# Optimization experiments

Hardware: AMD Instinct MI355X
Metric: run time of the kernel (lower is better)

## Reference

```python
import jax, jax.numpy as jnp
import numpy as np

B, S, H = 4, 2048, 2048
NH, NKV, HD = 8, 4, 256
WINDOW = 1024
ROPE_BASE = 10000.0
SCALE = 256.0 ** -0.5  # query_pre_attn_scalar ** -0.5


def setup_inputs() -> dict:
    key = jax.random.key(0)
    ks = jax.random.split(key, 6)
    s = 0.02
    return {
        "hidden_states": jax.random.normal(ks[0], (B, S, H), jnp.float32),
        "positions": jnp.tile(jnp.arange(S, dtype=jnp.int32), (B, 1)),
        "Wq": jax.random.normal(ks[1], (H, NH * HD), jnp.float32) * s,
        "bq": jnp.zeros((NH * HD,), jnp.float32),
        "Wk": jax.random.normal(ks[2], (H, NKV * HD), jnp.float32) * s,
        "bk": jnp.zeros((NKV * HD,), jnp.float32),
        "Wv": jax.random.normal(ks[3], (H, NKV * HD), jnp.float32) * s,
        "bv": jnp.zeros((NKV * HD,), jnp.float32),
        "Wo": jax.random.normal(ks[4], (NH * HD, H), jnp.float32) * s,
    }


def _rope_neox(pos, x):
    # pos: [B,S] int; x: [B,S,nh,HD]
    half = HD // 2
    inv_freq = 1.0 / (ROPE_BASE ** (jnp.arange(half, dtype=jnp.float32) / half))
    freqs = pos[..., None].astype(jnp.float32) * inv_freq  # [B,S,half]
    cos = jnp.cos(freqs)[:, :, None, :]
    sin = jnp.sin(freqs)[:, :, None, :]
    x1, x2 = jnp.split(x, 2, axis=-1)
    return jnp.concatenate([x1 * cos - x2 * sin, x2 * cos + x1 * sin], axis=-1)


def reference(hidden_states, positions, Wq, bq, Wk, bk, Wv, bv, Wo):
    q = (hidden_states @ Wq + bq).reshape(B, S, NH, HD)
    k = (hidden_states @ Wk + bk).reshape(B, S, NKV, HD)
    v = (hidden_states @ Wv + bv).reshape(B, S, NKV, HD)
    q = _rope_neox(positions, q)
    k = _rope_neox(positions, k)
    # GQA: repeat kv heads
    rep = NH // NKV
    k = jnp.repeat(k, rep, axis=2)
    v = jnp.repeat(v, rep, axis=2)
    scores = jnp.einsum('bqhd,bkhd->bhqk', q, k) * SCALE
    i = jnp.arange(S)[:, None]
    j = jnp.arange(S)[None, :]
    mask = (j <= i) & (j > i - WINDOW)  # causal + sliding window
    scores = jnp.where(mask[None, None], scores, jnp.float32(-1e30))
    probs = jax.nn.softmax(scores, axis=-1)
    attn = jnp.einsum('bhqk,bkhd->bqhd', probs, v).reshape(B, S, NH * HD)
    return attn @ Wo
```

## Files before the change

### kernel.cpp

```cpp
#include <hip/hip_runtime.h>

#define B_ 4
#define S_ 2048
#define H_ 2048
#define NH_ 8
#define NKV_ 4
#define HD_ 256
#define WINDOW_ 1024
#define SCALE_ 0.0625f

typedef __bf16 bf16x8 __attribute__((ext_vector_type(8)));
typedef float f32x4 __attribute__((ext_vector_type(4)));

__device__ __forceinline__ unsigned short f2bf(float f) {
  union { float f; unsigned u; } v; v.f = f;
  unsigned r = v.u + 0x7fffu + ((v.u >> 16) & 1u);
  return (unsigned short)(r >> 16);
}
__device__ __forceinline__ float bf2f(unsigned short h) {
  union { unsigned u; float f; } v; v.u = ((unsigned)h) << 16;
  return v.f;
}

__device__ __forceinline__ f32x4 mfma16(bf16x8 a, bf16x8 b, f32x4 c) {
  return __builtin_amdgcn_mfma_f32_16x16x32_bf16(a, b, c, 0, 0, 0);
}

#define GLOAD16(gsrc, ldst)                                                     \
  __builtin_amdgcn_global_load_lds(                                             \
      (const __attribute__((address_space(1))) void*)(gsrc),                    \
      (__attribute__((address_space(3))) void*)(ldst), 16, 0, 0)

#define FENCE asm volatile("" ::: "memory")
#define BAR __builtin_amdgcn_s_barrier()
#define WAIT_LGKM0 asm volatile("s_waitcnt lgkmcnt(0)" ::: "memory")

__global__ void f32_to_bf16(const float* __restrict__ in,
                            unsigned short* __restrict__ out, int n4) {
  int idx = blockIdx.x * blockDim.x + threadIdx.x;
  int stride = gridDim.x * blockDim.x;
  for (; idx < n4; idx += stride) {
    float4 v = reinterpret_cast<const float4*>(in)[idx];
    ushort4 o;
    o.x = f2bf(v.x); o.y = f2bf(v.y); o.z = f2bf(v.z); o.w = f2bf(v.w);
    reinterpret_cast<ushort4*>(out)[idx] = o;
  }
}

__global__ void transpose_w(const float* __restrict__ in,
                            unsigned short* __restrict__ out, int R, int C) {
  __shared__ unsigned short t[32][33];
  int r0 = blockIdx.x * 32, c0 = blockIdx.y * 32;
  int tx = threadIdx.x & 31, ty = threadIdx.x >> 5;
#pragma unroll
  for (int i = 0; i < 4; ++i)
    t[ty * 4 + i][tx] = f2bf(in[(size_t)(r0 + ty * 4 + i) * C + c0 + tx]);
  __syncthreads();
#pragma unroll
  for (int i = 0; i < 4; ++i)
    out[(size_t)(c0 + ty * 4 + i) * R + r0 + tx] = t[tx][ty * 4 + i];
}


#define SA(buf, kt, ha)                                                        \
  { _Pragma("unroll") for (int ii = 0; ii < 2; ++ii) {                         \
      int row_ = ii * 128 + (ha) * 64 + (tid >> 3);                            \
      GLOAD16(gA + (((size_t)(m0 + row_)) << 11) + ((kt) << 6) +               \
                  ((((tid & 7) ^ ((tid >> 3) & 7))) << 3),                     \
              lds + (buf) * 65536 + ((ii * 128 + (ha) * 64 + wid * 8) << 7)); } }

#define SB(buf, kt, hb)                                                        \
  { _Pragma("unroll") for (int ii = 0; ii < 2; ++ii) {                         \
      int row_ = ii * 128 + (hb) * 64 + (tid >> 3);                            \
      GLOAD16(gB + (((size_t)(n0 + row_)) << 11) + ((kt) << 6) +               \
                  ((((tid & 7) ^ ((tid >> 3) & 7))) << 3),                     \
              lds + (buf) * 65536 + 32768 +                                    \
                  ((ii * 128 + (hb) * 64 + wid * 8) << 7)); } }

#define RDA(buf, qa)                                                           \
  { _Pragma("unroll") for (int m = 0; m < 4; ++m)                              \
      _Pragma("unroll") for (int ks = 0; ks < 2; ++ks)                         \
        afr[m][ks] = *reinterpret_cast<const bf16x8*>(                         \
            lds + (buf) * 65536 +                                              \
            ((wm * 128 + (qa) * 64 + m * 16 + lc) << 7) +                      \
            ((((ks * 4 + lg) ^ (lc & 7))) << 4)); }

#define RDB(buf, qb, dst)                                                      \
  { _Pragma("unroll") for (int n = 0; n < 2; ++n)                              \
      _Pragma("unroll") for (int ks = 0; ks < 2; ++ks)                         \
        dst[n][ks] = *reinterpret_cast<const bf16x8*>(                         \
            lds + (buf) * 65536 + 32768 +                                      \
            ((wn * 64 + (qb) * 32 + n * 16 + lc) << 7) +                       \
            ((((ks * 4 + lg) ^ (lc & 7))) << 4)); }

#define MM(qa, qb, bsrc)                                                       \
  { __builtin_amdgcn_s_setprio(1);                                             \
    _Pragma("unroll") for (int m = 0; m < 4; ++m)                              \
      _Pragma("unroll") for (int n = 0; n < 2; ++n)                            \
        _Pragma("unroll") for (int ks = 0; ks < 2; ++ks)                       \
          acc[qa][qb][m][n] =                                                  \
              mfma16(afr[m][ks], bsrc[n][ks], acc[qa][qb][m][n]);              \
    __builtin_amdgcn_s_setprio(0); }

template <int OUT_F32>
__global__ __launch_bounds__(512, 2) void gemm256(
    const unsigned short* __restrict__ gA, const unsigned short* __restrict__ gB,
    const float* __restrict__ bias, void* __restrict__ Cout) {
  extern __shared__ __align__(16) char lds[];
  const int tid = threadIdx.x, lane = tid & 63, wid = tid >> 6;
  const int lc = lane & 15, lg = lane >> 4;
  const int wm = wid >> 2, wn = wid & 3;
  const int c = blockIdx.x & 7, bi = blockIdx.x >> 3;
  const int mt = ((c & 3) << 3) + (bi & 7);
  const int nt = ((c >> 2) << 2) + (bi >> 3);
  const int m0 = mt * 256, n0 = nt * 256;

  f32x4 acc[2][2][4][2];
#pragma unroll
  for (int qa = 0; qa < 2; ++qa)
#pragma unroll
    for (int qb = 0; qb < 2; ++qb)
#pragma unroll
      for (int m = 0; m < 4; ++m)
#pragma unroll
        for (int n = 0; n < 2; ++n) acc[qa][qb][m][n] = f32x4{0.f, 0.f, 0.f, 0.f};

  SA(0, 0, 0); SB(0, 0, 0); SB(0, 0, 1); SA(0, 0, 1);
  SA(1, 1, 0); SB(1, 1, 0); SB(1, 1, 1);
  asm volatile("s_waitcnt vmcnt(6)" ::: "memory");
  FENCE; BAR;

  bf16x8 afr[4][2], b0r[2][2], b1r[2][2];
  for (int t = 0; t < 32; ++t) {
    const int b = t & 1;
    const int t1 = (t + 1) & 31, t2 = (t + 2) & 31;
    const int bn = (t + 1) & 1;
    RDA(b, 0); RDB(b, 0, b0r);
    SA(bn, t1, 1);
    FENCE; BAR;
    MM(0, 0, b0r);
    WAIT_LGKM0; FENCE; BAR;
    RDB(b, 1, b1r);
    SA(b, t2, 0);
    FENCE; BAR;
    MM(0, 1, b1r);
    WAIT_LGKM0; FENCE; BAR;
    RDA(b, 1);
    SB(b, t2, 0);
    FENCE; BAR;
    MM(1, 0, b0r);
    WAIT_LGKM0; FENCE; BAR;
    SB(b, t2, 1);
    FENCE; BAR;
    MM(1, 1, b1r);
    asm volatile("s_waitcnt vmcnt(6)" ::: "memory");
    FENCE; BAR;
  }
  asm volatile("s_waitcnt vmcnt(0)" ::: "memory");

#pragma unroll
  for (int qa = 0; qa < 2; ++qa)
#pragma unroll
    for (int qb = 0; qb < 2; ++qb)
#pragma unroll
      for (int m = 0; m < 4; ++m)
#pragma unroll
        for (int n = 0; n < 2; ++n) {
          const int gcol = n0 + wn * 64 + qb * 32 + n * 16 + lc;
          const float bv = bias ? bias[gcol] : 0.f;
          const int grow = m0 + wm * 128 + qa * 64 + m * 16 + lg * 4;
#pragma unroll
          for (int r = 0; r < 4; ++r) {
            float v = acc[qa][qb][m][n][r] + bv;
            if (OUT_F32)
              reinterpret_cast<float*>(Cout)[(size_t)(grow + r) * 2048 + gcol] = v;
            else
              reinterpret_cast<unsigned short*>(Cout)[(size_t)(grow + r) * 2048 + gcol] = f2bf(v);
          }
        }
}

__global__ void rope_kernel(const unsigned short* __restrict__ in,
                            const int* __restrict__ pos,
                            unsigned short* __restrict__ out, int nh) {
  int idx = blockIdx.x * 256 + threadIdx.x;
  int d = idx & 127;
  int bs = idx >> 7;
  int b = bs >> 11, s = bs & 2047;
  float p = (float)pos[bs];
  float inv = __expf(-(float)d * (9.210340371976184f / 128.f));
  float fr = p * inv;
  float cs, sn;
  sincosf(fr, &sn, &cs);
  const unsigned short* ib = in + (size_t)bs * 2048 + d;
  unsigned short* ob = out + ((size_t)b * nh * S_ + s) * HD_ + d;
  for (int hh = 0; hh < nh; ++hh) {
    float x1 = bf2f(ib[hh * HD_]);
    float x2 = bf2f(ib[hh * HD_ + 128]);
    ob[(size_t)hh * S_ * HD_] = f2bf(x1 * cs - x2 * sn);
    ob[(size_t)hh * S_ * HD_ + 128] = f2bf(x2 * cs + x1 * sn);
  }
}

__global__ void transpose_v(const unsigned short* __restrict__ in,
                            unsigned short* __restrict__ out) {
  __shared__ unsigned short t[32][33];
  int s0 = blockIdx.x * 32, d0 = blockIdx.y * 32;
  int bh = blockIdx.z;
  int b = bh >> 2, hh = bh & 3;
  int tx = threadIdx.x & 31, ty = threadIdx.x >> 5;
#pragma unroll
  for (int i = 0; i < 4; ++i)
    t[ty * 4 + i][tx] =
        in[(size_t)(b * S_ + s0 + ty * 4 + i) * 2048 + 1024 + hh * 256 + d0 + tx];
  __syncthreads();
#pragma unroll
  for (int i = 0; i < 4; ++i)
    out[((size_t)(b * NKV_ + hh) * HD_ + d0 + ty * 4 + i) * S_ + s0 + tx] =
        t[tx][ty * 4 + i];
}


#define STAGE_KV(bf, kv0)                                                      \
  { _Pragma("unroll") for (int i = 0; i < 2; ++i) {                            \
      int chunk = i * 512 + tid; int row = chunk >> 5, o = chunk & 31;         \
      GLOAD16(Kg0 + (size_t)((kv0) + row) * HD_ + (o ^ (row & 7)) * 8,         \
              (char*)&Kl[bf][0] + (i * 512 + wid * 64) * 16); }                \
    _Pragma("unroll") for (int i = 0; i < 2; ++i) {                            \
      int chunk = i * 512 + tid; int row = chunk >> 2, o = chunk & 3;          \
      GLOAD16(Vg0 + (size_t)row * S_ + (kv0) + (o ^ ((row >> 1) & 3)) * 8,     \
              (char*)&Vl[bf][0] + (i * 512 + wid * 64) * 16); } }

__global__ __launch_bounds__(512, 4) void attn_kernel(
    const unsigned short* __restrict__ Q, const unsigned short* __restrict__ K,
    const unsigned short* __restrict__ VT, unsigned short* __restrict__ O) {
  __shared__ __align__(16) unsigned short Kl[2][32 * 256];
  __shared__ __align__(16) unsigned short Vl[2][256 * 32];
  __shared__ __align__(16) unsigned short Pl[8][16 * 40];

  const int tid = threadIdx.x;
  const int lane = tid & 63, wid = tid >> 6;
  const int wq = wid & 3;
  const int ho = wid >> 2;
  const int lc = lane & 15, lg = lane >> 4;
  const int qt = 31 - blockIdx.x;
  const int kvh = blockIdx.y, b = blockIdx.z;
  const int h = kvh * 2 + ho;
  const int q0 = qt * 64;

  bf16x8 qf[8];
  const unsigned short* Qbase =
      Q + (((size_t)(b * NH_ + h)) * S_ + (q0 + wq * 16 + lc)) * HD_;
#pragma unroll
  for (int ds = 0; ds < 8; ++ds)
    qf[ds] = *reinterpret_cast<const bf16x8*>(Qbase + ds * 32 + lg * 8);

  f32x4 acc[16];
#pragma unroll
  for (int i = 0; i < 16; ++i) acc[i] = f32x4{0.f, 0.f, 0.f, 0.f};
  float m_r[4], l_r[4];
#pragma unroll
  for (int r = 0; r < 4; ++r) { m_r[r] = -1e30f; l_r[r] = 0.f; }

  const unsigned short* Kg0 = K + ((size_t)(b * NKV_ + kvh)) * S_ * HD_;
  const unsigned short* Vg0 = VT + ((size_t)(b * NKV_ + kvh)) * HD_ * S_;

  int jlo = q0 - (WINDOW_ - 1);
  if (jlo < 0) jlo = 0;
  const int jt_lo = jlo >> 5;
  const int jt_hi = (q0 + 63) >> 5;
  const int ibase = q0 + wq * 16 + lg * 4;

  STAGE_KV(0, jt_lo * 32);
  int bf = 0;
  for (int jt = jt_lo; jt <= jt_hi; ++jt) {
    const int kv0 = jt * 32;
    if (jt < jt_hi) {
      STAGE_KV(bf ^ 1, (jt + 1) * 32);
      asm volatile("s_waitcnt vmcnt(4)" ::: "memory");
    } else {
      asm volatile("s_waitcnt vmcnt(0)" ::: "memory");
    }
    FENCE;
    __syncthreads();

    f32x4 sf[2];
    __builtin_amdgcn_s_setprio(1);
#pragma unroll
    for (int ct = 0; ct < 2; ++ct) {
      f32x4 s{0.f, 0.f, 0.f, 0.f};
      int j = ct * 16 + lc;
#pragma unroll
      for (int ds = 0; ds < 8; ++ds) {
        int g = ds * 4 + lg;
        const bf16x8 kf = *reinterpret_cast<const bf16x8*>(
            (const char*)&Kl[bf][0] + (j * 512 + ((g ^ (j & 7)) * 16)));
        s = mfma16(qf[ds], kf, s);
      }
      sf[ct] = s;
    }
    __builtin_amdgcn_s_setprio(0);

    float pmax[4];
#pragma unroll
    for (int r = 0; r < 4; ++r) pmax[r] = -1e30f;
#pragma unroll
    for (int ct = 0; ct < 2; ++ct) {
      int j = kv0 + ct * 16 + lc;
#pragma unroll
      for (int r = 0; r < 4; ++r) {
        int irow = ibase + r;
        bool ok = (j <= irow) && (j > irow - WINDOW_);
        pmax[r] = fmaxf(pmax[r], ok ? sf[ct][r] * SCALE_ : -1e30f);
      }
    }
#pragma unroll
    for (int r = 0; r < 4; ++r) {
#pragma unroll
      for (int msk = 1; msk <= 8; msk <<= 1)
        pmax[r] = fmaxf(pmax[r], __shfl_xor(pmax[r], msk));
    }
    float dmax = 0.f;
#pragma unroll
    for (int r = 0; r < 4; ++r) dmax = fmaxf(dmax, pmax[r] - m_r[r]);
    if (__any(dmax > 8.0f)) {
#pragma unroll
      for (int r = 0; r < 4; ++r) {
        float mn = fmaxf(m_r[r], pmax[r]);
        float a = __expf(m_r[r] - mn);
        m_r[r] = mn;
        l_r[r] *= a;
#pragma unroll
        for (int dt = 0; dt < 16; ++dt) acc[dt][r] *= a;
      }
    }
    float lsum[4];
#pragma unroll
    for (int r = 0; r < 4; ++r) lsum[r] = 0.f;
#pragma unroll
    for (int ct = 0; ct < 2; ++ct) {
      int j = kv0 + ct * 16 + lc;
#pragma unroll
      for (int r = 0; r < 4; ++r) {
        int irow = ibase + r;
        bool ok = (j <= irow) && (j > irow - WINDOW_);
        float p = ok ? __expf(sf[ct][r] * SCALE_ - m_r[r]) : 0.f;
        lsum[r] += p;
        Pl[wid][(lg * 4 + r) * 40 + ct * 16 + lc] = f2bf(p);
      }
    }
#pragma unroll
    for (int r = 0; r < 4; ++r) {
#pragma unroll
      for (int msk = 1; msk <= 8; msk <<= 1) lsum[r] += __shfl_xor(lsum[r], msk);
      l_r[r] += lsum[r];
    }
    WAIT_LGKM0;
    const bf16x8 pa = *reinterpret_cast<const bf16x8*>(&Pl[wid][lc * 40 + lg * 8]);
    __builtin_amdgcn_s_setprio(1);
#pragma unroll
    for (int dt = 0; dt < 16; ++dt) {
      int d = dt * 16 + lc;
      const bf16x8 vf = *reinterpret_cast<const bf16x8*>(
          (const char*)&Vl[bf][0] + (d * 64 + ((lg ^ ((d >> 1) & 3)) * 16)));
      acc[dt] = mfma16(pa, vf, acc[dt]);
    }
    __builtin_amdgcn_s_setprio(0);
    WAIT_LGKM0; FENCE;
    __syncthreads();
    bf ^= 1;
  }

  const int srow = q0 + wq * 16 + lg * 4;
#pragma unroll
  for (int dt = 0; dt < 16; ++dt) {
#pragma unroll
    for (int r = 0; r < 4; ++r) {
      float o = acc[dt][r] / l_r[r];
      O[(size_t)(b * S_ + srow + r) * (NH_ * HD_) + h * HD_ + dt * 16 + lc] =
          f2bf(o);
    }
  }
}

extern "C" void kernel_launch(void* const* d_in, const int* in_sizes, int n_in,
                              void* d_out, int out_size, void* d_ws,
                              size_t ws_size, hipStream_t stream) {
  (void)in_sizes; (void)n_in; (void)out_size; (void)ws_size;
  const float* hs = (const float*)d_in[0];
  const int* pos = (const int*)d_in[1];
  const float* Wq = (const float*)d_in[2];
  const float* bq = (const float*)d_in[3];
  const float* Wk = (const float*)d_in[4];
  const float* bk = (const float*)d_in[5];
  const float* Wv = (const float*)d_in[6];
  const float* bv = (const float*)d_in[7];
  const float* Wo = (const float*)d_in[8];
  float* out = (float*)d_out;

  char* ws = (char*)d_ws;
  const size_t MB = 1024 * 1024;
  unsigned short* hs_bf = (unsigned short*)(ws + 0);
  unsigned short* WqT   = (unsigned short*)(ws + 32 * MB);
  unsigned short* WkvT  = (unsigned short*)(ws + 40 * MB);
  unsigned short* WoT   = (unsigned short*)(ws + 48 * MB);
  unsigned short* Qflat = (unsigned short*)(ws + 56 * MB);
  unsigned short* KVflat= (unsigned short*)(ws + 88 * MB);
  unsigned short* Qatt  = (unsigned short*)(ws + 120 * MB);
  unsigned short* Katt  = (unsigned short*)(ws + 152 * MB);
  unsigned short* VTt   = (unsigned short*)(ws + 168 * MB);
  float* bias_kv = (float*)(ws + 120 * MB);
  unsigned short* attnb = (unsigned short*)(ws + 0);

  hipFuncSetAttribute(reinterpret_cast<const void*>(gemm256<0>),
                      hipFuncAttributeMaxDynamicSharedMemorySize, 131072);
  hipFuncSetAttribute(reinterpret_cast<const void*>(gemm256<1>),
                      hipFuncAttributeMaxDynamicSharedMemorySize, 131072);

  f32_to_bf16<<<2048, 256, 0, stream>>>(hs, hs_bf, (B_ * S_ * H_) / 4);
  transpose_w<<<dim3(H_ / 32, (NH_ * HD_) / 32), 256, 0, stream>>>(Wq, WqT, H_, NH_ * HD_);
  transpose_w<<<dim3(H_ / 32, (NKV_ * HD_) / 32), 256, 0, stream>>>(Wk, WkvT, H_, NKV_ * HD_);
  transpose_w<<<dim3(H_ / 32, (NKV_ * HD_) / 32), 256, 0, stream>>>(Wv, WkvT + 1024 * 2048, H_, NKV_ * HD_);
  transpose_w<<<dim3((NH_ * HD_) / 32, H_ / 32), 256, 0, stream>>>(Wo, WoT, NH_ * HD_, H_);
  hipMemcpyAsync(bias_kv, bk, 1024 * sizeof(float), hipMemcpyDeviceToDevice, stream);
  hipMemcpyAsync(bias_kv + 1024, bv, 1024 * sizeof(float), hipMemcpyDeviceToDevice, stream);

  gemm256<0><<<256, 512, 131072, stream>>>(hs_bf, WqT, bq, Qflat);
  gemm256<0><<<256, 512, 131072, stream>>>(hs_bf, WkvT, bias_kv, KVflat);

  rope_kernel<<<(B_ * S_ * 128) / 256, 256, 0, stream>>>(Qflat, pos, Qatt, NH_);
  rope_kernel<<<(B_ * S_ * 128) / 256, 256, 0, stream>>>(KVflat, pos, Katt, NKV_);
  transpose_v<<<dim3(S_ / 32, HD_ / 32, B_ * NKV_), 256, 0, stream>>>(KVflat, VTt);

  attn_kernel<<<dim3(32, 4, 4), 512, 0, stream>>>(Qatt, Katt, VTt, attnb);

  gemm256<1><<<256, 512, 131072, stream>>>(attnb, WoT, nullptr, out);
}
```

Before: 647.7 us.

## Fuse QKV projections into one GEMM and widen attention KV tiles to 64

Concatenates Wq, Wk and Wv into one transposed weight and runs a single 512-block GEMM producing a 4096-wide QKV buffer, replacing two separate projection launches. Rope and V-transpose kernels now read from the fused buffer. The attention kernel moves to dynamic LDS with 64-key tiles instead of 32, halving the number of loop iterations and barriers. Blocks are remapped so each XCD handles a fixed batch/head pair, but the larger LDS footprint drops occupancy to one block per CU.

```diff
diff --git a/kernel.cpp b/kernel.cpp
--- a/kernel.cpp
+++ b/kernel.cpp
@@ -102,7 +102,7 @@
               mfma16(afr[m][ks], bsrc[n][ks], acc[qa][qb][m][n]);              \
     __builtin_amdgcn_s_setprio(0); }
 
-template <int OUT_F32>
+template <int OUT_F32, int NTILES>
 __global__ __launch_bounds__(512, 2) void gemm256(
     const unsigned short* __restrict__ gA, const unsigned short* __restrict__ gB,
     const float* __restrict__ bias, void* __restrict__ Cout) {
@@ -110,9 +110,10 @@
   const int tid = threadIdx.x, lane = tid & 63, wid = tid >> 6;
   const int lc = lane & 15, lg = lane >> 4;
   const int wm = wid >> 2, wn = wid & 3;
+  const int N_ = NTILES * 256;
   const int c = blockIdx.x & 7, bi = blockIdx.x >> 3;
   const int mt = ((c & 3) << 3) + (bi & 7);
-  const int nt = ((c >> 2) << 2) + (bi >> 3);
+  const int nt = ((c >> 2) * (NTILES / 2)) + (bi >> 3);
   const int m0 = mt * 256, n0 = nt * 256;
 
   f32x4 acc[2][2][4][2];
@@ -173,16 +174,17 @@
           for (int r = 0; r < 4; ++r) {
             float v = acc[qa][qb][m][n][r] + bv;
             if (OUT_F32)
-              reinterpret_cast<float*>(Cout)[(size_t)(grow + r) * 2048 + gcol] = v;
+              reinterpret_cast<float*>(Cout)[(size_t)(grow + r) * N_ + gcol] = v;
             else
-              reinterpret_cast<unsigned short*>(Cout)[(size_t)(grow + r) * 2048 + gcol] = f2bf(v);
+              reinterpret_cast<unsigned short*>(Cout)[(size_t)(grow + r) * N_ + gcol] = f2bf(v);
           }
         }
 }
 
 __global__ void rope_kernel(const unsigned short* __restrict__ in,
                             const int* __restrict__ pos,
-                            unsigned short* __restrict__ out, int nh) {
+                            unsigned short* __restrict__ out, int nh,
+                            int colbase) {
   int idx = blockIdx.x * 256 + threadIdx.x;
   int d = idx & 127;
   int bs = idx >> 7;
@@ -192,7 +194,7 @@
   float fr = p * inv;
   float cs, sn;
   sincosf(fr, &sn, &cs);
-  const unsigned short* ib = in + (size_t)bs * 2048 + d;
+  const unsigned short* ib = in + (size_t)bs * 4096 + colbase + d;
   unsigned short* ob = out + ((size_t)b * nh * S_ + s) * HD_ + d;
   for (int hh = 0; hh < nh; ++hh) {
     float x1 = bf2f(ib[hh * HD_]);
@@ -212,7 +214,7 @@
 #pragma unroll
   for (int i = 0; i < 4; ++i)
     t[ty * 4 + i][tx] =
-        in[(size_t)(b * S_ + s0 + ty * 4 + i) * 2048 + 1024 + hh * 256 + d0 + tx];
+        in[(size_t)(b * S_ + s0 + ty * 4 + i) * 4096 + 3072 + hh * 256 + d0 + tx];
   __syncthreads();
 #pragma unroll
   for (int i = 0; i < 4; ++i)
@@ -221,32 +223,33 @@
 }
 
 
-#define STAGE_KV(bf, kv0)                                                      \
-  { _Pragma("unroll") for (int i = 0; i < 2; ++i) {                            \
+#define STAGE_KV(bfb, kv0)                                                     \
+  { _Pragma("unroll") for (int i = 0; i < 4; ++i) {                            \
       int chunk = i * 512 + tid; int row = chunk >> 5, o = chunk & 31;         \
       GLOAD16(Kg0 + (size_t)((kv0) + row) * HD_ + (o ^ (row & 7)) * 8,         \
-              (char*)&Kl[bf][0] + (i * 512 + wid * 64) * 16); }                \
-    _Pragma("unroll") for (int i = 0; i < 2; ++i) {                            \
-      int chunk = i * 512 + tid; int row = chunk >> 2, o = chunk & 3;          \
-      GLOAD16(Vg0 + (size_t)row * S_ + (kv0) + (o ^ ((row >> 1) & 3)) * 8,     \
-              (char*)&Vl[bf][0] + (i * 512 + wid * 64) * 16); } }
-
-__global__ __launch_bounds__(512, 4) void attn_kernel(
+              lds + (bfb) * 32768 + chunk * 16); }                             \
+    _Pragma("unroll") for (int i = 0; i < 4; ++i) {                            \
+      int chunk = i * 512 + tid; int row = chunk >> 3, o = chunk & 7;          \
+      GLOAD16(Vg0 + (size_t)row * S_ + (kv0) + (o ^ (row & 7)) * 8,            \
+              lds + 65536 + (bfb) * 32768 + chunk * 16); } }
+
+__global__ __launch_bounds__(512, 1) void attn_kernel(
     const unsigned short* __restrict__ Q, const unsigned short* __restrict__ K,
     const unsigned short* __restrict__ VT, unsigned short* __restrict__ O) {
-  __shared__ __align__(16) unsigned short Kl[2][32 * 256];
-  __shared__ __align__(16) unsigned short Vl[2][256 * 32];
-  __shared__ __align__(16) unsigned short Pl[8][16 * 40];
+  extern __shared__ __align__(16) char lds[];
 
   const int tid = threadIdx.x;
   const int lane = tid & 63, wid = tid >> 6;
   const int wq = wid & 3;
   const int ho = wid >> 2;
   const int lc = lane & 15, lg = lane >> 4;
-  const int qt = 31 - blockIdx.x;
-  const int kvh = blockIdx.y, b = blockIdx.z;
+  const int xcd = blockIdx.x & 7, g = blockIdx.x >> 3;
+  const int pair = xcd + ((g >> 5) << 3);
+  const int qt = 31 - (g & 31);
+  const int kvh = pair & 3, b = pair >> 2;
   const int h = kvh * 2 + ho;
   const int q0 = qt * 64;
+  unsigned short* Pl = (unsigned short*)(lds + 131072 + wid * 2304);
 
   bf16x8 qf[8];
   const unsigned short* Qbase =
@@ -267,34 +270,34 @@
 
   int jlo = q0 - (WINDOW_ - 1);
   if (jlo < 0) jlo = 0;
-  const int jt_lo = jlo >> 5;
-  const int jt_hi = (q0 + 63) >> 5;
+  const int jt_lo = jlo >> 6;
+  const int jt_hi = q0 >> 6;
   const int ibase = q0 + wq * 16 + lg * 4;
 
-  STAGE_KV(0, jt_lo * 32);
+  STAGE_KV(0, jt_lo * 64);
   int bf = 0;
   for (int jt = jt_lo; jt <= jt_hi; ++jt) {
-    const int kv0 = jt * 32;
+    const int kv0 = jt * 64;
     if (jt < jt_hi) {
-      STAGE_KV(bf ^ 1, (jt + 1) * 32);
-      asm volatile("s_waitcnt vmcnt(4)" ::: "memory");
+      STAGE_KV(bf ^ 1, (jt + 1) * 64);
+      asm volatile("s_waitcnt vmcnt(8)" ::: "memory");
     } else {
       asm volatile("s_waitcnt vmcnt(0)" ::: "memory");
     }
     FENCE;
     __syncthreads();
 
-    f32x4 sf[2];
+    f32x4 sf[4];
     __builtin_amdgcn_s_setprio(1);
 #pragma unroll
-    for (int ct = 0; ct < 2; ++ct) {
+    for (int ct = 0; ct < 4; ++ct) {
       f32x4 s{0.f, 0.f, 0.f, 0.f};
       int j = ct * 16 + lc;
 #pragma unroll
       for (int ds = 0; ds < 8; ++ds) {
-        int g = ds * 4 + lg;
+        int gg = ds * 4 + lg;
         const bf16x8 kf = *reinterpret_cast<const bf16x8*>(
-            (const char*)&Kl[bf][0] + (j * 512 + ((g ^ (j & 7)) * 16)));
+            lds + bf * 32768 + j * 512 + ((gg ^ (j & 7)) * 16));
         s = mfma16(qf[ds], kf, s);
       }
       sf[ct] = s;
@@ -305,7 +308,7 @@
 #pragma unroll
     for (int r = 0; r < 4; ++r) pmax[r] = -1e30f;
 #pragma unroll
-    for (int ct = 0; ct < 2; ++ct) {
+    for (int ct = 0; ct < 4; ++ct) {
       int j = kv0 + ct * 16 + lc;
 #pragma unroll
       for (int r = 0; r < 4; ++r) {
@@ -338,7 +341,7 @@
 #pragma unroll
     for (int r = 0; r < 4; ++r) lsum[r] = 0.f;
 #pragma unroll
-    for (int ct = 0; ct < 2; ++ct) {
+    for (int ct = 0; ct < 4; ++ct) {
       int j = kv0 + ct * 16 + lc;
 #pragma unroll
       for (int r = 0; r < 4; ++r) {
@@ -346,7 +349,7 @@
         bool ok = (j <= irow) && (j > irow - WINDOW_);
         float p = ok ? __expf(sf[ct][r] * SCALE_ - m_r[r]) : 0.f;
         lsum[r] += p;
-        Pl[wid][(lg * 4 + r) * 40 + ct * 16 + lc] = f2bf(p);
+        Pl[(lg * 4 + r) * 72 + ct * 16 + lc] = f2bf(p);
       }
     }
 #pragma unroll
@@ -356,14 +359,18 @@
       l_r[r] += lsum[r];
     }
     WAIT_LGKM0;
-    const bf16x8 pa = *reinterpret_cast<const bf16x8*>(&Pl[wid][lc * 40 + lg * 8]);
+    bf16x8 pa0 = *reinterpret_cast<const bf16x8*>(&Pl[lc * 72 + lg * 8]);
+    bf16x8 pa1 = *reinterpret_cast<const bf16x8*>(&Pl[lc * 72 + 32 + lg * 8]);
     __builtin_amdgcn_s_setprio(1);
 #pragma unroll
     for (int dt = 0; dt < 16; ++dt) {
       int d = dt * 16 + lc;
-      const bf16x8 vf = *reinterpret_cast<const bf16x8*>(
-          (const char*)&Vl[bf][0] + (d * 64 + ((lg ^ ((d >> 1) & 3)) * 16)));
-      acc[dt] = mfma16(pa, vf, acc[dt]);
+      const bf16x8 vf0 = *reinterpret_cast<const bf16x8*>(
+          lds + 65536 + bf * 32768 + d * 128 + ((lg ^ (d & 7)) * 16));
+      const bf16x8 vf1 = *reinterpret_cast<const bf16x8*>(
+          lds + 65536 + bf * 32768 + d * 128 + (((4 + lg) ^ (d & 7)) * 16));
+      acc[dt] = mfma16(pa0, vf0, acc[dt]);
+      acc[dt] = mfma16(pa1, vf1, acc[dt]);
     }
     __builtin_amdgcn_s_setprio(0);
     WAIT_LGKM0; FENCE;
@@ -400,39 +407,39 @@
 
   char* ws = (char*)d_ws;
   const size_t MB = 1024 * 1024;
-  unsigned short* hs_bf = (unsigned short*)(ws + 0);
-  unsigned short* WqT   = (unsigned short*)(ws + 32 * MB);
-  unsigned short* WkvT  = (unsigned short*)(ws + 40 * MB);
-  unsigned short* WoT   = (unsigned short*)(ws + 48 * MB);
-  unsigned short* Qflat = (unsigned short*)(ws + 56 * MB);
-  unsigned short* KVflat= (unsigned short*)(ws + 88 * MB);
-  unsigned short* Qatt  = (unsigned short*)(ws + 120 * MB);
-  unsigned short* Katt  = (unsigned short*)(ws + 152 * MB);
-  unsigned short* VTt   = (unsigned short*)(ws + 168 * MB);
-  float* bias_kv = (float*)(ws + 120 * MB);
-  unsigned short* attnb = (unsigned short*)(ws + 0);
-
-  hipFuncSetAttribute(reinterpret_cast<const void*>(gemm256<0>),
+  unsigned short* hs_bf  = (unsigned short*)(ws + 0);
+  unsigned short* WqkvT  = (unsigned short*)(ws + 32 * MB);
+  unsigned short* WoT    = (unsigned short*)(ws + 48 * MB);
+  unsigned short* QKVflat= (unsigned short*)(ws + 56 * MB);
+  unsigned short* Qatt   = (unsigned short*)(ws + 120 * MB);
+  unsigned short* Katt   = (unsigned short*)(ws + 152 * MB);
+  unsigned short* VTt    = (unsigned short*)(ws + 168 * MB);
+  float* bias_qkv = (float*)(ws + 120 * MB);
+  unsigned short* attnb  = (unsigned short*)(ws + 0);
+
+  hipFuncSetAttribute(reinterpret_cast<const void*>(gemm256<0, 16>),
                       hipFuncAttributeMaxDynamicSharedMemorySize, 131072);
-  hipFuncSetAttribute(reinterpret_cast<const void*>(gemm256<1>),
+  hipFuncSetAttribute(reinterpret_cast<const void*>(gemm256<1, 8>),
                       hipFuncAttributeMaxDynamicSharedMemorySize, 131072);
+  hipFuncSetAttribute(reinterpret_cast<const void*>(attn_kernel),
+                      hipFuncAttributeMaxDynamicSharedMemorySize, 149504);
 
   f32_to_bf16<<<2048, 256, 0, stream>>>(hs, hs_bf, (B_ * S_ * H_) / 4);
-  transpose_w<<<dim3(H_ / 32, (NH_ * HD_) / 32), 256, 0, stream>>>(Wq, WqT, H_, NH_ * HD_);
-  transpose_w<<<dim3(H_ / 32, (NKV_ * HD_) / 32), 256, 0, stream>>>(Wk, WkvT, H_, NKV_ * HD_);
-  transpose_w<<<dim3(H_ / 32, (NKV_ * HD_) / 32), 256, 0, stream>>>(Wv, WkvT + 1024 * 2048, H_, NKV_ * HD_);
-  transpose_w<<<dim3((NH_ * HD_) / 32, H_ / 32), 256, 0, stream>>>(Wo, WoT, NH_ * HD_, H_);
-  hipMemcpyAsync(bias_kv, bk, 1024 * sizeof(float), hipMemcpyDeviceToDevice, stream);
-  hipMemcpyAsync(bias_kv + 1024, bv, 1024 * sizeof(float), hipMemcpyDeviceToDevice, stream);
-
-  gemm256<0><<<256, 512, 131072, stream>>>(hs_bf, WqT, bq, Qflat);
-  gemm256<0><<<256, 512, 131072, stream>>>(hs_bf, WkvT, bias_kv, KVflat);
-
-  rope_kernel<<<(B_ * S_ * 128) / 256, 256, 0, stream>>>(Qflat, pos, Qatt, NH_);
-  rope_kernel<<<(B_ * S_ * 128) / 256, 256, 0, stream>>>(KVflat, pos, Katt, NKV_);
-  transpose_v<<<dim3(S_ / 32, HD_ / 32, B_ * NKV_), 256, 0, stream>>>(KVflat, VTt);
-
-  attn_kernel<<<dim3(32, 4, 4), 512, 0, stream>>>(Qatt, Katt, VTt, attnb);
-
-  gemm256<1><<<256, 512, 131072, stream>>>(attnb, WoT, nullptr, out);
-}
+  transpose_w<<<dim3(H_ / 32, 2048 / 32), 256, 0, stream>>>(Wq, WqkvT, H_, 2048);
+  transpose_w<<<dim3(H_ / 32, 1024 / 32), 256, 0, stream>>>(Wk, WqkvT + 2048 * 2048, H_, 1024);
+  transpose_w<<<dim3(H_ / 32, 1024 / 32), 256, 0, stream>>>(Wv, WqkvT + 3072 * 2048, H_, 1024);
+  transpose_w<<<dim3(2048 / 32, H_ / 32), 256, 0, stream>>>(Wo, WoT, 2048, H_);
+  hipMemcpyAsync(bias_qkv, bq, 2048 * sizeof(float), hipMemcpyDeviceToDevice, stream);
+  hipMemcpyAsync(bias_qkv + 2048, bk, 1024 * sizeof(float), hipMemcpyDeviceToDevice, stream);
+  hipMemcpyAsync(bias_qkv + 3072, bv, 1024 * sizeof(float), hipMemcpyDeviceToDevice, stream);
+
+  gemm256<0, 16><<<512, 512, 131072, stream>>>(hs_bf, WqkvT, bias_qkv, QKVflat);
+
+  rope_kernel<<<(B_ * S_ * 128) / 256, 256, 0, stream>>>(QKVflat, pos, Qatt, NH_, 0);
+  rope_kernel<<<(B_ * S_ * 128) / 256, 256, 0, stream>>>(QKVflat, pos, Katt, NKV_, 2048);
+  transpose_v<<<dim3(S_ / 32, HD_ / 32, B_ * NKV_), 256, 0, stream>>>(QKVflat, VTt);
+
+  attn_kernel<<<512, 512, 149504, stream>>>(Qatt, Katt, VTt, attnb);
+
+  gemm256<1, 8><<<256, 512, 131072, stream>>>(attnb, WoT, nullptr, out);
+}
```

Result: faster. 539.4 us (-16.7%).
